# Performance work log

Hardware: AMD Instinct MI355X
Metric: run time of the kernel (lower is better)

Reference implementation:

```python
import jax, jax.numpy as jnp
import numpy as np

N_EMBD = 1024
N_HEAD = 16


def setup_inputs() -> dict:
    key = jax.random.key(0)
    ks = jax.random.split(key, 5)
    C = N_EMBD
    x = jax.random.normal(ks[0], (4, 2048, C), dtype=jnp.float32)
    s = 1.0 / np.sqrt(C)
    W_attn = jax.random.normal(ks[1], (C, 3 * C), dtype=jnp.float32) * s
    b_attn = jnp.zeros((3 * C,), dtype=jnp.float32)
    W_proj = jax.random.normal(ks[2], (C, C), dtype=jnp.float32) * s
    b_proj = jnp.zeros((C,), dtype=jnp.float32)
    return {"x": x, "W_attn": W_attn, "b_attn": b_attn, "W_proj": W_proj, "b_proj": b_proj}


def reference(x, W_attn, b_attn, W_proj, b_proj):
    B, T, C = x.shape
    H = N_HEAD
    D = C // H
    qkv = x @ W_attn + b_attn                      # [B,T,3C]
    q, k, v = jnp.split(qkv, 3, axis=-1)
    # [B,H,T,D]
    q = q.reshape(B, T, H, D).transpose(0, 2, 1, 3)
    k = k.reshape(B, T, H, D).transpose(0, 2, 1, 3)
    v = v.reshape(B, T, H, D).transpose(0, 2, 1, 3)
    scale = 1.0 / jnp.sqrt(jnp.asarray(D, dtype=x.dtype))
    att = jnp.einsum('bhqd,bhkd->bhqk', q, k) * scale   # [B,H,T,T]
    causal = jnp.tril(jnp.ones((T, T), dtype=bool))
    att = jnp.where(causal, att, jnp.finfo(att.dtype).min)
    att = jax.nn.softmax(att, axis=-1)
    y = jnp.einsum('bhqk,bhkd->bhqd', att, v)            # [B,H,T,D]
    y = y.transpose(0, 2, 1, 3).reshape(B, T, C)
    return y @ W_proj + b_proj
```

## Files before the change

kernel.cpp:

```cpp
#include <hip/hip_runtime.h>
#include <type_traits>

typedef __attribute__((ext_vector_type(8))) short short8;
typedef __attribute__((ext_vector_type(8))) unsigned short ushort8;
typedef __attribute__((ext_vector_type(4))) float floatx4;

__device__ __forceinline__ unsigned short f2bf(float f) {
    union { float f; unsigned int i; } v;
    v.f = f;
    unsigned int u = v.i;
    unsigned int r = (u + 0x7FFFu + ((u >> 16) & 1u)) >> 16;
    return (unsigned short)r;
}

__device__ __forceinline__ void gload_lds16(const unsigned short* g, unsigned short* lds_base) {
    __builtin_amdgcn_global_load_lds(
        (const __attribute__((address_space(1))) unsigned int*)g,
        (__attribute__((address_space(3))) unsigned int*)lds_base,
        16, 0, 0);
}

__global__ __launch_bounds__(256) void cvt_f32_bf16_kernel(
    const float* __restrict__ src, unsigned short* __restrict__ dst, int n8)
{
    int i = blockIdx.x * 256 + threadIdx.x;
    if (i >= n8) return;
    const float4* s = (const float4*)src + (size_t)i * 2;
    float4 a = s[0];
    float4 b = s[1];
    ushort8 r;
    r[0] = f2bf(a.x); r[1] = f2bf(a.y); r[2] = f2bf(a.z); r[3] = f2bf(a.w);
    r[4] = f2bf(b.x); r[5] = f2bf(b.y); r[6] = f2bf(b.z); r[7] = f2bf(b.w);
    *((ushort8*)dst + i) = r;
}

__global__ __launch_bounds__(256) void transpose_cvt_kernel(
    const float* __restrict__ src, unsigned short* __restrict__ dst, int K, int N)
{
    __shared__ float tile[32][33];
    const int tx = threadIdx.x & 31;
    const int ty = threadIdx.x >> 5;
    const int k0 = blockIdx.y * 32, n0 = blockIdx.x * 32;
#pragma unroll
    for (int i = 0; i < 4; ++i)
        tile[ty + i * 8][tx] = src[(size_t)(k0 + ty + i * 8) * N + n0 + tx];
    __syncthreads();
#pragma unroll
    for (int i = 0; i < 4; ++i)
        dst[(size_t)(n0 + ty + i * 8) * K + k0 + tx] = f2bf(tile[tx][ty + i * 8]);
}

template <int MODE, typename OutT>
__global__ __launch_bounds__(256) void gemm128_kernel(
    const unsigned short* __restrict__ A,
    const unsigned short* __restrict__ Bt,
    const float* __restrict__ bias,
    OutT* __restrict__ C,
    unsigned short* __restrict__ Qo,
    unsigned short* __restrict__ Ko,
    unsigned short* __restrict__ Vto,
    int M, int N, int K)
{
    __shared__ __align__(16) unsigned short As[128 * 32];
    __shared__ __align__(16) unsigned short Bs[128 * 32];

    const int tid  = threadIdx.x;
    const int lane = tid & 63;
    const int w    = tid >> 6;
    const int wm   = w & 1;
    const int wn   = w >> 1;
    const int quad = lane >> 4;
    const int l16  = lane & 15;

    const int m0 = blockIdx.y * 128;
    const int n0 = blockIdx.x * 128;

    floatx4 acc[4][4];
#pragma unroll
    for (int i = 0; i < 4; ++i)
#pragma unroll
        for (int j = 0; j < 4; ++j) acc[i][j] = (floatx4)0.0f;

    const int r0 = tid >> 2;
    const int kc = (tid & 3) << 3;
    const unsigned short* Ag = A  + (size_t)(m0 + r0) * K + kc;
    const unsigned short* Bg = Bt + (size_t)(n0 + r0) * K + kc;
    unsigned short* AsW = As + w * 512;
    unsigned short* BsW = Bs + w * 512;

    for (int k0 = 0; k0 < K; k0 += 32) {
        __syncthreads();
#pragma unroll
        for (int i = 0; i < 2; ++i) {
            gload_lds16(Ag + (size_t)(i * 64) * K + k0, AsW + i * 2048);
            gload_lds16(Bg + (size_t)(i * 64) * K + k0, BsW + i * 2048);
        }
        __syncthreads();

        short8 a[4], b[4];
#pragma unroll
        for (int mi = 0; mi < 4; ++mi)
            a[mi] = *(const short8*)&As[(wm * 64 + mi * 16 + l16) * 32 + (quad << 3)];
#pragma unroll
        for (int ni = 0; ni < 4; ++ni)
            b[ni] = *(const short8*)&Bs[(wn * 64 + ni * 16 + l16) * 32 + (quad << 3)];
#pragma unroll
        for (int mi = 0; mi < 4; ++mi)
#pragma unroll
            for (int ni = 0; ni < 4; ++ni)
                acc[mi][ni] = __builtin_amdgcn_mfma_f32_16x16x32_bf16(a[mi], b[ni], acc[mi][ni], 0, 0, 0);
    }

#pragma unroll
    for (int ni = 0; ni < 4; ++ni) {
        const int n = n0 + wn * 64 + ni * 16 + l16;
        const float bval = bias[n];
        const int seg = n >> 10;
        const int nl  = n & 1023;
#pragma unroll
        for (int mi = 0; mi < 4; ++mi) {
            if constexpr (MODE == 0) {
#pragma unroll
                for (int r = 0; r < 4; ++r) {
                    const int m = m0 + wm * 64 + mi * 16 + (quad << 2) + r;
                    const float val = acc[mi][ni][r] + bval;
                    if constexpr (std::is_same<OutT, unsigned short>::value)
                        C[(size_t)m * N + n] = f2bf(val);
                    else
                        C[(size_t)m * N + n] = val;
                }
            } else {
                if (seg < 2) {
                    unsigned short* P = (seg == 0) ? Qo : Ko;
#pragma unroll
                    for (int r = 0; r < 4; ++r) {
                        const int m = m0 + wm * 64 + mi * 16 + (quad << 2) + r;
                        P[(size_t)m * 1024 + nl] = f2bf(acc[mi][ni][r] + bval);
                    }
                } else {
                    const int mb = m0 + wm * 64 + mi * 16 + (quad << 2);
                    const int bb = mb >> 11, t0 = mb & 2047;
                    unsigned int lo = (unsigned int)f2bf(acc[mi][ni][0] + bval) |
                                      ((unsigned int)f2bf(acc[mi][ni][1] + bval) << 16);
                    unsigned int hi = (unsigned int)f2bf(acc[mi][ni][2] + bval) |
                                      ((unsigned int)f2bf(acc[mi][ni][3] + bval) << 16);
                    uint2 pv; pv.x = lo; pv.y = hi;
                    *(uint2*)(Vto + ((size_t)bb * 1024 + nl) * 2048 + t0) = pv;
                }
            }
        }
    }
}

__global__ __launch_bounds__(256, 8) void attn_kernel(
    const unsigned short* __restrict__ Q,
    const unsigned short* __restrict__ Kq,
    const unsigned short* __restrict__ Vt,
    unsigned short* __restrict__ Y)
{
    const int T = 2048;

    int idx = blockIdx.x;
    int qt  = 31 - (idx >> 6);
    int bh  = idx & 63;
    int b   = bh >> 4;
    int h   = bh & 15;

    const int tid  = threadIdx.x;
    const int lane = tid & 63;
    const int w    = tid >> 6;
    const int quad = lane >> 4;
    const int l16  = lane & 15;

    __shared__ __align__(16) unsigned short Ks2[8 * 64 * 8];
    __shared__ __align__(16) unsigned short Vs2[8 * 64 * 8];
    __shared__ __align__(16) unsigned short Ps[4][16][72];

    const unsigned short* qp =
        Q + (size_t)(b * T + qt * 64 + (w << 4) + l16) * 1024 + h * 64;
    short8 qf0 = *(const short8*)(qp + (quad << 3));
    short8 qf1 = *(const short8*)(qp + 32 + (quad << 3));

    float l_run = 0.0f;
    floatx4 o[4];
#pragma unroll
    for (int ns = 0; ns < 4; ++ns) o[ns] = (floatx4)0.0f;

    const unsigned short* kg0p = Kq + (size_t)(b * T + lane) * 1024 + h * 64 + (w) * 8;
    const unsigned short* kg1p = Kq + (size_t)(b * T + lane) * 1024 + h * 64 + (w + 4) * 8;
    const unsigned short* vg0p = Vt + ((size_t)(b * 1024 + h * 64 + lane)) * 2048 + (w) * 8;
    const unsigned short* vg1p = Vt + ((size_t)(b * 1024 + h * 64 + lane)) * 2048 + (w + 4) * 8;

    const int qg_local = (w << 4) + l16;

    const float SC2 = 0.18033688011112042f;
    const float MB2 = -17.312340490667562f;

    const int ktiles = qt + 1;
    for (int kt = 0; kt < ktiles; ++kt) {
        const int key0 = kt << 6;
        __syncthreads();
        gload_lds16(kg0p + (size_t)key0 * 1024, Ks2 + (w) * 512);
        gload_lds16(kg1p + (size_t)key0 * 1024, Ks2 + (w + 4) * 512);
        gload_lds16(vg0p + key0, Vs2 + (w) * 512);
        gload_lds16(vg1p + key0, Vs2 + (w + 4) * 512);
        __syncthreads();

        floatx4 s[4];
#pragma unroll
        for (int ks = 0; ks < 4; ++ks) {
            s[ks] = (floatx4)0.0f;
            short8 kf0 = *(const short8*)&Ks2[((0 * 4 + quad) * 64 + ks * 16 + l16) * 8];
            short8 kf1 = *(const short8*)&Ks2[((1 * 4 + quad) * 64 + ks * 16 + l16) * 8];
            s[ks] = __builtin_amdgcn_mfma_f32_16x16x32_bf16(kf0, qf0, s[ks], 0, 0, 0);
            s[ks] = __builtin_amdgcn_mfma_f32_16x16x32_bf16(kf1, qf1, s[ks], 0, 0, 0);
        }

        if (kt < qt) {
#pragma unroll
            for (int ks = 0; ks < 4; ++ks) {
                float pv0 = __builtin_amdgcn_exp2f(fmaf(s[ks][0], SC2, MB2));
                float pv1 = __builtin_amdgcn_exp2f(fmaf(s[ks][1], SC2, MB2));
                float pv2 = __builtin_amdgcn_exp2f(fmaf(s[ks][2], SC2, MB2));
                float pv3 = __builtin_amdgcn_exp2f(fmaf(s[ks][3], SC2, MB2));
                l_run += (pv0 + pv1) + (pv2 + pv3);
                unsigned int lo, hi;
                asm("v_cvt_pk_bf16_f32 %0, %1, %2" : "=v"(lo) : "v"(pv0), "v"(pv1));
                asm("v_cvt_pk_bf16_f32 %0, %1, %2" : "=v"(hi) : "v"(pv2), "v"(pv3));
                uint2 pk; pk.x = lo; pk.y = hi;
                *(uint2*)&Ps[w][l16][(ks << 4) + (quad << 2)] = pk;
            }
        } else {
            const int kq4 = quad << 2;
#pragma unroll
            for (int ks = 0; ks < 4; ++ks) {
                const int kb = (ks << 4) + kq4;
                float a0 = (kb + 0 <= qg_local) ? fmaf(s[ks][0], SC2, MB2) : -100000.0f;
                float a1 = (kb + 1 <= qg_local) ? fmaf(s[ks][1], SC2, MB2) : -100000.0f;
                float a2 = (kb + 2 <= qg_local) ? fmaf(s[ks][2], SC2, MB2) : -100000.0f;
                float a3 = (kb + 3 <= qg_local) ? fmaf(s[ks][3], SC2, MB2) : -100000.0f;
                float pv0 = __builtin_amdgcn_exp2f(a0);
                float pv1 = __builtin_amdgcn_exp2f(a1);
                float pv2 = __builtin_amdgcn_exp2f(a2);
                float pv3 = __builtin_amdgcn_exp2f(a3);
                l_run += (pv0 + pv1) + (pv2 + pv3);
                unsigned int lo, hi;
                asm("v_cvt_pk_bf16_f32 %0, %1, %2" : "=v"(lo) : "v"(pv0), "v"(pv1));
                asm("v_cvt_pk_bf16_f32 %0, %1, %2" : "=v"(hi) : "v"(pv2), "v"(pv3));
                uint2 pk; pk.x = lo; pk.y = hi;
                *(uint2*)&Ps[w][l16][(ks << 4) + (quad << 2)] = pk;
            }
        }

        short8 pf0 = *(const short8*)&Ps[w][l16][quad << 3];
        short8 pf1 = *(const short8*)&Ps[w][l16][32 + (quad << 3)];
#pragma unroll
        for (int ns = 0; ns < 4; ++ns) {
            short8 vf0 = *(const short8*)&Vs2[((0 * 4 + quad) * 64 + ns * 16 + l16) * 8];
            short8 vf1 = *(const short8*)&Vs2[((1 * 4 + quad) * 64 + ns * 16 + l16) * 8];
            o[ns] = __builtin_amdgcn_mfma_f32_16x16x32_bf16(pf0, vf0, o[ns], 0, 0, 0);
            o[ns] = __builtin_amdgcn_mfma_f32_16x16x32_bf16(pf1, vf1, o[ns], 0, 0, 0);
        }
    }

    float ssum = l_run;
    ssum += __shfl_xor(ssum, 16, 64);
    ssum += __shfl_xor(ssum, 32, 64);
    const float linv = 1.0f / ssum;
    float li[4];
#pragma unroll
    for (int r = 0; r < 4; ++r) li[r] = __shfl(linv, (quad << 2) + r, 64);

#pragma unroll
    for (int ns = 0; ns < 4; ++ns) {
        int d = (ns << 4) + l16;
#pragma unroll
        for (int r = 0; r < 4; ++r) {
            int t = qt * 64 + (w << 4) + (quad << 2) + r;
            Y[(size_t)(b * T + t) * 1024 + h * 64 + d] = f2bf(o[ns][r] * li[r]);
        }
    }
}

extern "C" void kernel_launch(void* const* d_in, const int* in_sizes, int n_in,
                              void* d_out, int out_size, void* d_ws, size_t ws_size,
                              hipStream_t stream) {
    const float* x  = (const float*)d_in[0];
    const float* Wa = (const float*)d_in[1];
    const float* ba = (const float*)d_in[2];
    const float* Wp = (const float*)d_in[3];
    const float* bp = (const float*)d_in[4];
    float* out = (float*)d_out;

    const size_t NX = (size_t)8192 * 1024;

    unsigned short* Qb  = (unsigned short*)d_ws;
    unsigned short* Kb  = Qb  + NX;
    unsigned short* Vtb = Kb  + NX;
    unsigned short* Yb  = Vtb + NX;
    unsigned short* xb  = Yb  + NX;
    unsigned short* Wat = xb  + NX;
    unsigned short* Wpt = Wat + (size_t)3072 * 1024;

    cvt_f32_bf16_kernel<<<(int)(NX / 8 / 256), 256, 0, stream>>>(x, xb, (int)(NX / 8));
    transpose_cvt_kernel<<<dim3(3072 / 32, 1024 / 32), 256, 0, stream>>>(Wa, Wat, 1024, 3072);
    transpose_cvt_kernel<<<dim3(1024 / 32, 1024 / 32), 256, 0, stream>>>(Wp, Wpt, 1024, 1024);

    gemm128_kernel<1, unsigned short><<<dim3(3072 / 128, 8192 / 128), 256, 0, stream>>>(
        xb, Wat, ba, (unsigned short*)nullptr, Qb, Kb, Vtb, 8192, 3072, 1024);

    attn_kernel<<<4 * 16 * (2048 / 64), 256, 0, stream>>>(Qb, Kb, Vtb, Yb);

    gemm128_kernel<0, float><<<dim3(1024 / 128, 8192 / 128), 256, 0, stream>>>(
        Yb, Wpt, bp, out, nullptr, nullptr, nullptr, 8192, 1024, 1024);
}
```

Baseline: 271.2 us.

## Replace 128x128 GEMM with double-buffered 256x256 pipelined GEMM with XCD-aware block mapping

Both projection GEMMs now use a 512-thread kernel computing 256x256 tiles with K-step 64. The kernel double-buffers LDS, interleaves global-to-LDS loads with MFMA phases under fine-grained barriers and waitcnts, and raises wave priority during MFMA bursts. Block IDs are remapped so that consecutive tiles land on the same XCD, which should improve L2 reuse. The aim is to hide load latency and raise arithmetic intensity. In exchange the kernel carries heavy register pressure from 32 accumulators and gets fewer workgroups, for example only 128 blocks for the output projection.

```diff
diff --git a/kernel.cpp b/kernel.cpp
--- a/kernel.cpp
+++ b/kernel.cpp
@@ -18,6 +18,12 @@
         (const __attribute__((address_space(1))) unsigned int*)g,
         (__attribute__((address_space(3))) unsigned int*)lds_base,
         16, 0, 0);
+}
+
+__device__ __forceinline__ void pbar() {
+    asm volatile("" ::: "memory");
+    __builtin_amdgcn_s_barrier();
+    asm volatile("" ::: "memory");
 }
 
 __global__ __launch_bounds__(256) void cvt_f32_bf16_kernel(
@@ -51,7 +57,7 @@
 }
 
 template <int MODE, typename OutT>
-__global__ __launch_bounds__(256) void gemm128_kernel(
+__global__ __launch_bounds__(512, 2) void gemm256_kernel(
     const unsigned short* __restrict__ A,
     const unsigned short* __restrict__ Bt,
     const float* __restrict__ bias,
@@ -59,57 +65,150 @@
     unsigned short* __restrict__ Qo,
     unsigned short* __restrict__ Ko,
     unsigned short* __restrict__ Vto,
-    int M, int N, int K)
+    int M, int N, int K, int gx)
 {
-    __shared__ __align__(16) unsigned short As[128 * 32];
-    __shared__ __align__(16) unsigned short Bs[128 * 32];
+    __shared__ __align__(16) unsigned short As[2][8][256][8];
+    __shared__ __align__(16) unsigned short Bs[2][8][256][8];
 
     const int tid  = threadIdx.x;
     const int lane = tid & 63;
     const int w    = tid >> 6;
-    const int wm   = w & 1;
-    const int wn   = w >> 1;
+    const int wm   = w >> 2;
+    const int wn   = w & 3;
     const int quad = lane >> 4;
     const int l16  = lane & 15;
 
-    const int m0 = blockIdx.y * 128;
-    const int n0 = blockIdx.x * 128;
-
-    floatx4 acc[4][4];
-#pragma unroll
-    for (int i = 0; i < 4; ++i)
+    const int nwg = gridDim.x;
+    const int cpx = nwg >> 3;
+    const int bid = blockIdx.x;
+    const int wg  = (bid & 7) * cpx + (bid >> 3);
+    const int by  = wg / gx;
+    const int bx  = wg - by * gx;
+    const int m0  = by << 8;
+    const int n0  = bx << 8;
+
+    floatx4 acc[8][4];
+#pragma unroll
+    for (int i = 0; i < 8; ++i)
 #pragma unroll
         for (int j = 0; j < 4; ++j) acc[i][j] = (floatx4)0.0f;
 
-    const int r0 = tid >> 2;
-    const int kc = (tid & 3) << 3;
-    const unsigned short* Ag = A  + (size_t)(m0 + r0) * K + kc;
-    const unsigned short* Bg = Bt + (size_t)(n0 + r0) * K + kc;
-    unsigned short* AsW = As + w * 512;
-    unsigned short* BsW = Bs + w * 512;
-
-    for (int k0 = 0; k0 < K; k0 += 32) {
-        __syncthreads();
-#pragma unroll
-        for (int i = 0; i < 2; ++i) {
-            gload_lds16(Ag + (size_t)(i * 64) * K + k0, AsW + i * 2048);
-            gload_lds16(Bg + (size_t)(i * 64) * K + k0, BsW + i * 2048);
-        }
-        __syncthreads();
-
-        short8 a[4], b[4];
-#pragma unroll
-        for (int mi = 0; mi < 4; ++mi)
-            a[mi] = *(const short8*)&As[(wm * 64 + mi * 16 + l16) * 32 + (quad << 3)];
+    const unsigned short* Agl = A  + ((size_t)m0 + lane) * K + w * 8;
+    const unsigned short* Bgl = Bt + ((size_t)n0 + lane) * K + w * 8;
+
+#define STA(buf, t, q) gload_lds16(Agl + (size_t)((q) * 64) * K + (t) * 64, &As[buf][w][(q) * 64][0])
+#define STB(buf, t, q) gload_lds16(Bgl + (size_t)((q) * 64) * K + (t) * 64, &Bs[buf][w][(q) * 64][0])
+
+    const int nt = K >> 6;
+
+#pragma unroll
+    for (int q = 0; q < 4; ++q) STB(0, 0, q);
+#pragma unroll
+    for (int q = 0; q < 4; ++q) STA(0, 0, q);
+#pragma unroll
+    for (int q = 0; q < 4; ++q) STB(1, 1, q);
+    asm volatile("s_waitcnt vmcnt(4)" ::: "memory");
+    pbar();
+
+    const int rA = wm * 128 + l16;
+    const int rB = wn * 64 + l16;
+
+    for (int h = 0; h < nt; ++h) {
+        const int b = h & 1;
+
+        short8 bfr[4][2];
 #pragma unroll
         for (int ni = 0; ni < 4; ++ni)
-            b[ni] = *(const short8*)&Bs[(wn * 64 + ni * 16 + l16) * 32 + (quad << 3)];
-#pragma unroll
-        for (int mi = 0; mi < 4; ++mi)
+#pragma unroll
+            for (int kc = 0; kc < 2; ++kc)
+                bfr[ni][kc] = *(const short8*)&Bs[b][kc * 4 + quad][rB + ni * 16][0];
+        short8 a0[2][2];
+#pragma unroll
+        for (int x = 0; x < 2; ++x)
+#pragma unroll
+            for (int kc = 0; kc < 2; ++kc)
+                a0[x][kc] = *(const short8*)&As[b][kc * 4 + quad][rA + x * 16][0];
+        if (h + 1 < nt) {
+#pragma unroll
+            for (int q = 0; q < 4; ++q) STA(b ^ 1, h + 1, q);
+        }
+        asm volatile("s_waitcnt lgkmcnt(8)");
+        pbar();
+        asm volatile("s_waitcnt lgkmcnt(0)" ::: "memory");
+        __builtin_amdgcn_s_setprio(1);
+#pragma unroll
+        for (int x = 0; x < 2; ++x)
 #pragma unroll
             for (int ni = 0; ni < 4; ++ni)
-                acc[mi][ni] = __builtin_amdgcn_mfma_f32_16x16x32_bf16(a[mi], b[ni], acc[mi][ni], 0, 0, 0);
+#pragma unroll
+                for (int kc = 0; kc < 2; ++kc)
+                    acc[x][ni] = __builtin_amdgcn_mfma_f32_16x16x32_bf16(a0[x][kc], bfr[ni][kc], acc[x][ni], 0, 0, 0);
+        __builtin_amdgcn_s_setprio(0);
+        pbar();
+
+        short8 a1[2][2];
+#pragma unroll
+        for (int x = 0; x < 2; ++x)
+#pragma unroll
+            for (int kc = 0; kc < 2; ++kc)
+                a1[x][kc] = *(const short8*)&As[b][kc * 4 + quad][rA + (2 + x) * 16][0];
+        if (h + 2 < nt) { STB(b, h + 2, 0); STB(b, h + 2, 1); }
+        pbar();
+        asm volatile("s_waitcnt lgkmcnt(0)" ::: "memory");
+        __builtin_amdgcn_s_setprio(1);
+#pragma unroll
+        for (int x = 0; x < 2; ++x)
+#pragma unroll
+            for (int ni = 0; ni < 4; ++ni)
+#pragma unroll
+                for (int kc = 0; kc < 2; ++kc)
+                    acc[2 + x][ni] = __builtin_amdgcn_mfma_f32_16x16x32_bf16(a1[x][kc], bfr[ni][kc], acc[2 + x][ni], 0, 0, 0);
+        __builtin_amdgcn_s_setprio(0);
+        pbar();
+
+        short8 a2[2][2];
+#pragma unroll
+        for (int x = 0; x < 2; ++x)
+#pragma unroll
+            for (int kc = 0; kc < 2; ++kc)
+                a2[x][kc] = *(const short8*)&As[b][kc * 4 + quad][rA + (4 + x) * 16][0];
+        if (h + 2 < nt) { STB(b, h + 2, 2); STB(b, h + 2, 3); }
+        pbar();
+        asm volatile("s_waitcnt lgkmcnt(0)" ::: "memory");
+        __builtin_amdgcn_s_setprio(1);
+#pragma unroll
+        for (int x = 0; x < 2; ++x)
+#pragma unroll
+            for (int ni = 0; ni < 4; ++ni)
+#pragma unroll
+                for (int kc = 0; kc < 2; ++kc)
+                    acc[4 + x][ni] = __builtin_amdgcn_mfma_f32_16x16x32_bf16(a2[x][kc], bfr[ni][kc], acc[4 + x][ni], 0, 0, 0);
+        __builtin_amdgcn_s_setprio(0);
+        pbar();
+
+        short8 a3[2][2];
+#pragma unroll
+        for (int x = 0; x < 2; ++x)
+#pragma unroll
+            for (int kc = 0; kc < 2; ++kc)
+                a3[x][kc] = *(const short8*)&As[b][kc * 4 + quad][rA + (6 + x) * 16][0];
+        pbar();
+        asm volatile("s_waitcnt lgkmcnt(0)" ::: "memory");
+        __builtin_amdgcn_s_setprio(1);
+#pragma unroll
+        for (int x = 0; x < 2; ++x)
+#pragma unroll
+            for (int ni = 0; ni < 4; ++ni)
+#pragma unroll
+                for (int kc = 0; kc < 2; ++kc)
+                    acc[6 + x][ni] = __builtin_amdgcn_mfma_f32_16x16x32_bf16(a3[x][kc], bfr[ni][kc], acc[6 + x][ni], 0, 0, 0);
+        __builtin_amdgcn_s_setprio(0);
+        if (h < nt - 2)       asm volatile("s_waitcnt vmcnt(4)" ::: "memory");
+        else if (h == nt - 2) asm volatile("s_waitcnt vmcnt(0)" ::: "memory");
+        pbar();
     }
+#undef STA
+#undef STB
 
 #pragma unroll
     for (int ni = 0; ni < 4; ++ni) {
@@ -118,11 +217,11 @@
         const int seg = n >> 10;
         const int nl  = n & 1023;
 #pragma unroll
-        for (int mi = 0; mi < 4; ++mi) {
+        for (int mi = 0; mi < 8; ++mi) {
             if constexpr (MODE == 0) {
 #pragma unroll
                 for (int r = 0; r < 4; ++r) {
-                    const int m = m0 + wm * 64 + mi * 16 + (quad << 2) + r;
+                    const int m = m0 + wm * 128 + mi * 16 + (quad << 2) + r;
                     const float val = acc[mi][ni][r] + bval;
                     if constexpr (std::is_same<OutT, unsigned short>::value)
                         C[(size_t)m * N + n] = f2bf(val);
@@ -134,11 +233,11 @@
                     unsigned short* P = (seg == 0) ? Qo : Ko;
 #pragma unroll
                     for (int r = 0; r < 4; ++r) {
-                        const int m = m0 + wm * 64 + mi * 16 + (quad << 2) + r;
+                        const int m = m0 + wm * 128 + mi * 16 + (quad << 2) + r;
                         P[(size_t)m * 1024 + nl] = f2bf(acc[mi][ni][r] + bval);
                     }
                 } else {
-                    const int mb = m0 + wm * 64 + mi * 16 + (quad << 2);
+                    const int mb = m0 + wm * 128 + mi * 16 + (quad << 2);
                     const int bb = mb >> 11, t0 = mb & 2047;
                     unsigned int lo = (unsigned int)f2bf(acc[mi][ni][0] + bval) |
                                       ((unsigned int)f2bf(acc[mi][ni][1] + bval) << 16);
@@ -306,11 +405,11 @@
     transpose_cvt_kernel<<<dim3(3072 / 32, 1024 / 32), 256, 0, stream>>>(Wa, Wat, 1024, 3072);
     transpose_cvt_kernel<<<dim3(1024 / 32, 1024 / 32), 256, 0, stream>>>(Wp, Wpt, 1024, 1024);
 
-    gemm128_kernel<1, unsigned short><<<dim3(3072 / 128, 8192 / 128), 256, 0, stream>>>(
-        xb, Wat, ba, (unsigned short*)nullptr, Qb, Kb, Vtb, 8192, 3072, 1024);
+    gemm256_kernel<1, unsigned short><<<dim3((8192 / 256) * (3072 / 256)), 512, 0, stream>>>(
+        xb, Wat, ba, (unsigned short*)nullptr, Qb, Kb, Vtb, 8192, 3072, 1024, 3072 / 256);
 
     attn_kernel<<<4 * 16 * (2048 / 64), 256, 0, stream>>>(Qb, Kb, Vtb, Yb);
 
-    gemm128_kernel<0, float><<<dim3(1024 / 128, 8192 / 128), 256, 0, stream>>>(
-        Yb, Wpt, bp, out, nullptr, nullptr, nullptr, 8192, 1024, 1024);
-}
+    gemm256_kernel<0, float><<<dim3((8192 / 256) * (1024 / 256)), 512, 0, stream>>>(
+        Yb, Wpt, bp, out, nullptr, nullptr, nullptr, 8192, 1024, 1024, 1024 / 256);
+}
```

Measured after the change: 331.1 us. 1.22x slower.
